# Kernel tuning notes

Hardware: AMD Instinct MI355X
Metric: run time of the kernel (lower is better)

The kernel has to match this reference:

```python
import jax, jax.numpy as jnp
import numpy as np

NUM_HEADS = 12


def setup_inputs() -> dict:
    key = jax.random.key(0)
    k1, k2, k3, k4 = jax.random.split(key, 4)
    dim = 768
    B, N1, N2 = 8, 64, 4096  # N1 must equal head_dim = dim // num_heads
    x = jax.random.normal(k1, (B, N1, dim), dtype=jnp.float32)
    y = jax.random.normal(k2, (B, N2, dim), dtype=jnp.float32)
    # torch nn.Linear layout: [out_features, in_features]
    W_qkv = jax.random.normal(k3, (3 * dim, dim), dtype=jnp.float32) * 0.02
    W_proj = jax.random.normal(k4, (dim, dim), dtype=jnp.float32) * 0.02
    b_proj = jnp.zeros((dim,), dtype=jnp.float32)
    return {"x": x, "y": y, "W_qkv": W_qkv, "W_proj": W_proj, "b_proj": b_proj}


def _split_heads(t, H):
    # [B, N, C] -> [B, H, N, C//H]
    B, N, C = t.shape
    return t.reshape(B, N, H, C // H).transpose(0, 2, 1, 3)


def reference(x, y, W_qkv, W_proj, b_proj):
    H = NUM_HEADS
    B1, N1, C = x.shape
    B2, N2, _ = y.shape
    hd = C // H
    scale = hd ** -0.5

    # qkv projections (bias=False); take q from x, k/v from y
    qkv_x = x @ W_qkv.T                      # [B, N1, 3C]
    q = _split_heads(qkv_x[..., :C], H)      # [B, H, N1, hd]
    qkv_y = y @ W_qkv.T                      # [B, N2, 3C]
    k = _split_heads(qkv_y[..., C:2 * C], H)  # [B, H, N2, hd]
    v = _split_heads(qkv_y[..., 2 * C:], H)   # [B, H, N2, hd]

    attn = jnp.einsum('bhqd,bhkd->bhqk', q, k) * scale  # [B, H, N1, N2]
    attn = jax.nn.softmax(attn, axis=-1)
    attn_t = attn.transpose(0, 1, 3, 2)       # [B, H, N2, N1]; N1 == hd

    # non-standard elementwise combine with v (requires N1 == hd)
    out = attn_t * v                          # [B, H, N2, hd]
    out = out.transpose(0, 2, 1, 3).reshape(B2, N2, C)
    return out @ W_proj.T + b_proj
```

## Files before the change

### kernel.cpp

```cpp
#include <hip/hip_runtime.h>
#include <math.h>


typedef __attribute__((ext_vector_type(8))) short short8;
typedef __attribute__((ext_vector_type(4))) float f32x4;

__device__ __forceinline__ ushort f2bf(float x) {
  unsigned u = __float_as_uint(x);
  u += 0x7fffu + ((u >> 16) & 1u);
  return (ushort)(u >> 16);
}
__device__ __forceinline__ float bf2f(ushort h) {
  return __uint_as_float((unsigned)h << 16);
}

__device__ __forceinline__ void gl_lds16(const ushort* g, ushort* l) {
  __builtin_amdgcn_global_load_lds(
      (__attribute__((address_space(1))) void*)g,
      (__attribute__((address_space(3))) void*)l, 16, 0, 0);
}

__global__ __launch_bounds__(256) void cast_all(
    const float* __restrict__ x, ushort* __restrict__ xb,
    const float* __restrict__ w1, ushort* __restrict__ w1b,
    const float* __restrict__ w2, ushort* __restrict__ w2b,
    const float* __restrict__ y, ushort* __restrict__ yb) {
  long i = (long)(blockIdx.x * 256 + threadIdx.x) * 8;
  if (i >= 27918336L) return;
  const float* s; ushort* d; long off;
  if (i < 393216L)        { s = x;  d = xb;  off = i; }
  else if (i < 2162688L)  { s = w1; d = w1b; off = i - 393216L; }
  else if (i < 2752512L)  { s = w2; d = w2b; off = i - 2162688L; }
  else                    { s = y;  d = yb;  off = i - 2752512L; }
  float4 a = *(const float4*)(s + off);
  float4 b = *(const float4*)(s + off + 4);
  ushort o[8] = {f2bf(a.x), f2bf(a.y), f2bf(a.z), f2bf(a.w),
                 f2bf(b.x), f2bf(b.y), f2bf(b.z), f2bf(b.w)};
  *(uint4*)(d + off) = *(const uint4*)o;
}

template <typename CT>
__device__ __forceinline__ void gemm8_body(
    const ushort* __restrict__ A, int lda,
    const ushort* __restrict__ B, int ldb,
    CT* __restrict__ C, int ldc,
    const float* __restrict__ bias, int rt, int ct)
{
  constexpr int NK = 12;
  __shared__ __align__(16) ushort Abuf[2][16384];
  __shared__ __align__(16) ushort Bbuf[2][16384];
  const int tid = threadIdx.x;
  const int m0 = rt * 256, n0 = ct * 256;
  const int wv = tid >> 6, lane = tid & 63;
  const int lm = lane & 15, quad = lane >> 4;
  const int WR = (wv >> 2) * 128, WC = (wv & 3) * 64;

  const int srow = lane >> 3;
  const int sg = (lane & 7) ^ srow;
  const ushort* Ag[4];
  const ushort* Bg[4];
#pragma unroll
  for (int j = 0; j < 4; ++j) {
    const int r = (wv * 4 + j) * 8 + srow;
    Ag[j] = A + (size_t)(m0 + r) * lda + sg * 8;
    Bg[j] = B + (size_t)(n0 + r) * ldb + sg * 8;
  }

  f32x4 acc[8][4];
#pragma unroll
  for (int i = 0; i < 8; ++i)
#pragma unroll
    for (int j = 0; j < 4; ++j) acc[i][j] = (f32x4)(0.f);

#pragma unroll
  for (int j = 0; j < 4; ++j) gl_lds16(Ag[j], &Abuf[0][(wv * 4 + j) * 512]);
#pragma unroll
  for (int j = 0; j < 4; ++j) gl_lds16(Bg[j], &Bbuf[0][(wv * 4 + j) * 512]);
#pragma unroll
  for (int j = 0; j < 4; ++j) gl_lds16(Bg[j] + 64, &Bbuf[1][(wv * 4 + j) * 512]);
  asm volatile("s_waitcnt vmcnt(4)" ::: "memory");
  __builtin_amdgcn_s_barrier();

#pragma unroll 1
  for (int T = 0; T < NK; ++T) {
    const ushort* Ab = &Abuf[T & 1][0];
    const ushort* Bb = &Bbuf[T & 1][0];
    ushort* An = &Abuf[(T & 1) ^ 1][0];
    ushort* Bn = &Bbuf[T & 1][0];
    const int k1 = (T + 1) * 64, k2 = (T + 2) * 64;
    const bool stA = (T + 1 < NK), stB = (T + 2 < NK);
    short8 bfr[4][2];

#pragma unroll
    for (int q = 0; q < 4; ++q) {
      if (q == 0) {
#pragma unroll
        for (int n = 0; n < 4; ++n)
#pragma unroll
          for (int ks = 0; ks < 2; ++ks)
            bfr[n][ks] = *(const short8*)(const void*)(
                Bb + (WC + n * 16 + lm) * 64 + ((ks * 4 + quad) ^ (lm & 7)) * 8);
      }
      short8 af[2][2];
#pragma unroll
      for (int i = 0; i < 2; ++i)
#pragma unroll
        for (int ks = 0; ks < 2; ++ks)
          af[i][ks] = *(const short8*)(const void*)(
              Ab + (WR + (q * 2 + i) * 16 + lm) * 64 + ((ks * 4 + quad) ^ (lm & 7)) * 8);
      if (q == 0 && stA) { gl_lds16(Ag[0] + k1, An + (wv * 4 + 0) * 512);
                           gl_lds16(Ag[1] + k1, An + (wv * 4 + 1) * 512); }
      if (q == 1 && stA) { gl_lds16(Ag[2] + k1, An + (wv * 4 + 2) * 512);
                           gl_lds16(Ag[3] + k1, An + (wv * 4 + 3) * 512); }
      if (q == 2 && stB) { gl_lds16(Bg[0] + k2, Bn + (wv * 4 + 0) * 512);
                           gl_lds16(Bg[1] + k2, Bn + (wv * 4 + 1) * 512); }
      if (q == 3 && stB) { gl_lds16(Bg[2] + k2, Bn + (wv * 4 + 2) * 512);
                           gl_lds16(Bg[3] + k2, Bn + (wv * 4 + 3) * 512); }
      __builtin_amdgcn_s_barrier();
      __builtin_amdgcn_s_setprio(1);
#pragma unroll
      for (int i = 0; i < 2; ++i)
#pragma unroll
        for (int n = 0; n < 4; ++n)
#pragma unroll
          for (int ks = 0; ks < 2; ++ks)
            acc[q * 2 + i][n] = __builtin_amdgcn_mfma_f32_16x16x32_bf16(
                af[i][ks], bfr[n][ks], acc[q * 2 + i][n], 0, 0, 0);
      __builtin_amdgcn_s_setprio(0);
      if (q == 3) {
        if (stB) asm volatile("s_waitcnt vmcnt(4)" ::: "memory");
        else     asm volatile("s_waitcnt vmcnt(0)" ::: "memory");
      }
      __builtin_amdgcn_s_barrier();
    }
  }
  __syncthreads();

  if constexpr (sizeof(CT) == 2) {
    ushort* eb = ((ushort*)&Abuf[0][0]) + wv * 2048;
#pragma unroll
    for (int i = 0; i < 8; ++i) {
      ushort* ebc = eb + (i & 1) * 1024;
#pragma unroll
      for (int j = 0; j < 4; ++j)
#pragma unroll
        for (int r = 0; r < 4; ++r) {
          const int R = quad * 4 + r;
          const int gt = j * 2 + (lm >> 3);
          const int gs = (gt + R) & 7;
          ebc[R * 64 + gs * 8 + (lm & 7)] = f2bf(acc[i][j][r]);
        }
#pragma unroll
      for (int p = 0; p < 2; ++p) {
        const int R2 = (lane >> 3) + p * 8;
        const int g = lane & 7;
        const int gt2 = (g - R2) & 7;
        uint4 v = *(const uint4*)(const void*)(ebc + R2 * 64 + g * 8);
        *(uint4*)(C + (size_t)(m0 + WR + i * 16 + R2) * ldc + n0 + WC + gt2 * 8) = v;
      }
    }
  } else {
#pragma unroll
    for (int j = 0; j < 4; ++j) {
      const int col = n0 + WC + j * 16 + lm;
      const float bb = bias ? bias[col] : 0.f;
#pragma unroll
      for (int i = 0; i < 8; ++i) {
        const int row = m0 + WR + i * 16 + quad * 4;
#pragma unroll
        for (int r = 0; r < 4; ++r)
          C[(size_t)(row + r) * ldc + col] = (CT)(acc[i][j][r] + bb);
      }
    }
  }
}

__global__ __launch_bounds__(512, 2) void kv_gemm8(
    const ushort* __restrict__ ybf, const ushort* __restrict__ wkv,
    ushort* __restrict__ kvbf)
{
  const int id = blockIdx.x;
  const int xcd = id & 7, local = id >> 3;
  const int rt = xcd * 16 + (local & 15);
  const int ct = local >> 4;
  gemm8_body<ushort>(ybf, 768, wkv, 768, kvbf, 1536, nullptr, rt, ct);
}

__global__ __launch_bounds__(512, 2) void out_gemm8(
    const ushort* __restrict__ Ebf, const ushort* __restrict__ wpbf,
    const float* __restrict__ bias, float* __restrict__ out)
{
  const int id = blockIdx.x;
  const int xcd = id & 7, local = id >> 3;
  const int rt = xcd * 16 + (local & 15);
  const int ct = local >> 4;
  gemm8_body<float>(Ebf, 768, wpbf, 768, out, 768, bias, rt, ct);
}

__global__ __launch_bounds__(256) void q_gemm(
    const ushort* __restrict__ A, const ushort* __restrict__ B,
    ushort* __restrict__ C)
{
  constexpr int lda = 768, ldb = 768, ldc = 768, K = 768;
  __shared__ __align__(16) ushort As[2][4096];
  __shared__ __align__(16) ushort Bs[2][4096];
  const int tid = threadIdx.x;
  const int rt = blockIdx.x & 3, ct = blockIdx.x >> 2;
  const int m0 = rt * 128, n0 = ct * 128;

  const int w = tid >> 6, lane = tid & 63;
  const int lm = lane & 15, quad = lane >> 4;
  const int wm = (w & 1) * 64, wn = (w >> 1) * 64;

  const int G0 = w * 64 + lane, G1 = G0 + 256;
  const int r0 = G0 >> 2, c0 = ((G0 & 3) - (r0 >> 1)) & 3;
  const int r1 = G1 >> 2, c1 = ((G1 & 3) - (r1 >> 1)) & 3;
  const ushort* Ag0 = A + (size_t)(m0 + r0) * lda + c0 * 8;
  const ushort* Ag1 = A + (size_t)(m0 + r1) * lda + c1 * 8;
  const ushort* Bg0 = B + (size_t)(n0 + r0) * ldb + c0 * 8;
  const ushort* Bg1 = B + (size_t)(n0 + r1) * ldb + c1 * 8;
  const int lds0 = w * 512, lds1 = w * 512 + 2048;

  f32x4 acc[4][4];
#pragma unroll
  for (int i = 0; i < 4; ++i)
#pragma unroll
    for (int j = 0; j < 4; ++j) acc[i][j] = (f32x4)(0.f);

  const int nk = K >> 5;
  gl_lds16(Ag0, &As[0][lds0]); gl_lds16(Ag1, &As[0][lds1]);
  gl_lds16(Bg0, &Bs[0][lds0]); gl_lds16(Bg1, &Bs[0][lds1]);

  int cur = 0;
  for (int kk = 0; kk < nk; ++kk) {
    __syncthreads();
    if (kk + 1 < nk) {
      const int k0 = (kk + 1) << 5;
      gl_lds16(Ag0 + k0, &As[cur ^ 1][lds0]); gl_lds16(Ag1 + k0, &As[cur ^ 1][lds1]);
      gl_lds16(Bg0 + k0, &Bs[cur ^ 1][lds0]); gl_lds16(Bg1 + k0, &Bs[cur ^ 1][lds1]);
    }
    const ushort* Ab = &As[cur][0];
    const ushort* Bb = &Bs[cur][0];
    short8 af[4], bf8[4];
#pragma unroll
    for (int i = 0; i < 4; ++i) {
      const int Ra = wm + i * 16 + lm;
      af[i] = *(const short8*)(const void*)(Ab + Ra * 32 + ((quad + (Ra >> 1)) & 3) * 8);
      const int Rb = wn + i * 16 + lm;
      bf8[i] = *(const short8*)(const void*)(Bb + Rb * 32 + ((quad + (Rb >> 1)) & 3) * 8);
    }
#pragma unroll
    for (int i = 0; i < 4; ++i)
#pragma unroll
      for (int j = 0; j < 4; ++j)
        acc[i][j] = __builtin_amdgcn_mfma_f32_16x16x32_bf16(af[i], bf8[j], acc[i][j], 0, 0, 0);
    cur ^= 1;
  }
  __syncthreads();

  ushort* eb = ((ushort*)&Bs[0][0]) + w * 2048;
#pragma unroll
  for (int i = 0; i < 4; ++i) {
    ushort* ebc = eb + (i & 1) * 1024;
#pragma unroll
    for (int j = 0; j < 4; ++j)
#pragma unroll
      for (int r = 0; r < 4; ++r) {
        const int R = quad * 4 + r;
        const int gt = j * 2 + (lm >> 3);
        const int gs = (gt + R) & 7;
        ebc[R * 64 + gs * 8 + (lm & 7)] = f2bf(acc[i][j][r]);
      }
#pragma unroll
    for (int p = 0; p < 2; ++p) {
      const int R2 = (lane >> 3) + p * 8;
      const int g = lane & 7;
      const int gt2 = (g - R2) & 7;
      uint4 v = *(const uint4*)(const void*)(ebc + R2 * 64 + g * 8);
      *(uint4*)(C + (size_t)(m0 + wm + i * 16 + R2) * ldc + n0 + wn + gt2 * 8) = v;
    }
  }
}

__global__ __launch_bounds__(256) void attn_pass1(
    const ushort* __restrict__ Q,
    const ushort* __restrict__ KV,
    float* __restrict__ parts)
{
  const int chunk = blockIdx.x, h = blockIdx.y, b = blockIdx.z;
  const int tid = threadIdx.x;
  __shared__ __align__(16) ushort Qs[64 * 72];
  __shared__ __align__(16) ushort Ks[128 * 72];
  __shared__ float sm[4][64], ss[4][64];
#pragma unroll
  for (int p = 0; p < 2; ++p) {
    const int G = tid + 256 * p, row = G >> 3, g = G & 7;
    *(uint4*)(Qs + row * 72 + g * 8) =
        *(const uint4*)(Q + (size_t)(b * 64 + row) * 768 + h * 64 + g * 8);
  }
#pragma unroll
  for (int p = 0; p < 4; ++p) {
    const int G = tid + 256 * p, row = G >> 3, g = G & 7;
    *(uint4*)(Ks + row * 72 + g * 8) =
        *(const uint4*)(KV + (size_t)(b * 4096 + chunk * 128 + row) * 1536 + h * 64 + g * 8);
  }
  __syncthreads();

  const int w = tid >> 6, lane = tid & 63;
  const int lm = lane & 15, quad = lane >> 4;
  const int wn = w * 32;

  f32x4 acc[4][2];
#pragma unroll
  for (int i = 0; i < 4; ++i) { acc[i][0] = (f32x4)(0.f); acc[i][1] = (f32x4)(0.f); }
#pragma unroll
  for (int s = 0; s < 2; ++s) {
    short8 qf[4], kf[2];
#pragma unroll
    for (int i = 0; i < 4; ++i)
      qf[i] = *(const short8*)(const void*)(Qs + (i * 16 + lm) * 72 + s * 32 + quad * 8);
#pragma unroll
    for (int jn = 0; jn < 2; ++jn)
      kf[jn] = *(const short8*)(const void*)(Ks + (wn + jn * 16 + lm) * 72 + s * 32 + quad * 8);
#pragma unroll
    for (int i = 0; i < 4; ++i)
#pragma unroll
      for (int jn = 0; jn < 2; ++jn)
        acc[i][jn] = __builtin_amdgcn_mfma_f32_16x16x32_bf16(qf[i], kf[jn], acc[i][jn], 0, 0, 0);
  }

#pragma unroll
  for (int i = 0; i < 4; ++i)
#pragma unroll
    for (int r = 0; r < 4; ++r) {
      float v0 = acc[i][0][r] * 0.125f, v1 = acc[i][1][r] * 0.125f;
      float m = fmaxf(v0, v1);
      m = fmaxf(m, __shfl_xor(m, 1)); m = fmaxf(m, __shfl_xor(m, 2));
      m = fmaxf(m, __shfl_xor(m, 4)); m = fmaxf(m, __shfl_xor(m, 8));
      float e = __expf(v0 - m) + __expf(v1 - m);
      e += __shfl_xor(e, 1); e += __shfl_xor(e, 2);
      e += __shfl_xor(e, 4); e += __shfl_xor(e, 8);
      if (lm == 0) {
        const int j = i * 16 + quad * 4 + r;
        sm[w][j] = m; ss[w][j] = e;
      }
    }
  __syncthreads();
  if (tid < 64) {
    float g = fmaxf(fmaxf(sm[0][tid], sm[1][tid]), fmaxf(sm[2][tid], sm[3][tid]));
    float s = ss[0][tid] * __expf(sm[0][tid] - g) + ss[1][tid] * __expf(sm[1][tid] - g)
            + ss[2][tid] * __expf(sm[2][tid] - g) + ss[3][tid] * __expf(sm[3][tid] - g);
    const int bh = b * 12 + h;
    float* p = parts + ((size_t)(bh * 32 + chunk) * 64 + tid) * 2;
    p[0] = g; p[1] = s;
  }
}

__global__ __launch_bounds__(256) void attn_pass2(
    const ushort* __restrict__ Q, const ushort* __restrict__ KV,
    const float* __restrict__ parts, ushort* __restrict__ E)
{
  const int chunk = blockIdx.x, h = blockIdx.y, b = blockIdx.z;
  const int tid = threadIdx.x;
  __shared__ __align__(16) ushort Qs[64 * 72];
  __shared__ __align__(16) ushort Ks[128 * 72];
  __shared__ __align__(16) ushort Vs[128 * 72];
  __shared__ float st[64][2];
#pragma unroll
  for (int p = 0; p < 2; ++p) {
    const int G = tid + 256 * p, row = G >> 3, g = G & 7;
    *(uint4*)(Qs + row * 72 + g * 8) =
        *(const uint4*)(Q + (size_t)(b * 64 + row) * 768 + h * 64 + g * 8);
  }
#pragma unroll
  for (int p = 0; p < 4; ++p) {
    const int G = tid + 256 * p, row = G >> 3, g = G & 7;
    const size_t rbase = (size_t)(b * 4096 + chunk * 128 + row) * 1536 + h * 64 + g * 8;
    *(uint4*)(Ks + row * 72 + g * 8) = *(const uint4*)(KV + rbase);
    *(uint4*)(Vs + row * 72 + g * 8) = *(const uint4*)(KV + rbase + 768);
  }
  {
    const int bh = b * 12 + h;
    const int tq = tid >> 2, tc = tid & 3;
    float pm[8], ps[8];
    float gm = -1e30f;
#pragma unroll
    for (int c = 0; c < 8; ++c) {
      const float* p = parts + ((size_t)(bh * 32 + tc * 8 + c) * 64 + tq) * 2;
      pm[c] = p[0]; ps[c] = p[1];
      gm = fmaxf(gm, pm[c]);
    }
    gm = fmaxf(gm, __shfl_xor(gm, 1));
    gm = fmaxf(gm, __shfl_xor(gm, 2));
    float s = 0.f;
#pragma unroll
    for (int c = 0; c < 8; ++c) s += ps[c] * __expf(pm[c] - gm);
    s += __shfl_xor(s, 1);
    s += __shfl_xor(s, 2);
    if (tc == 0) { st[tq][0] = gm; st[tq][1] = 1.f / s; }
  }
  __syncthreads();

  const int w = tid >> 6, lane = tid & 63;
  const int lm = lane & 15, quad = lane >> 4;
  const int wn = w * 32;

  f32x4 acc[4][2];
#pragma unroll
  for (int i = 0; i < 4; ++i) { acc[i][0] = (f32x4)(0.f); acc[i][1] = (f32x4)(0.f); }
#pragma unroll
  for (int s = 0; s < 2; ++s) {
    short8 qf[4], kf[2];
#pragma unroll
    for (int i = 0; i < 4; ++i)
      qf[i] = *(const short8*)(const void*)(Qs + (i * 16 + lm) * 72 + s * 32 + quad * 8);
#pragma unroll
    for (int jn = 0; jn < 2; ++jn)
      kf[jn] = *(const short8*)(const void*)(Ks + (wn + jn * 16 + lm) * 72 + s * 32 + quad * 8);
#pragma unroll
    for (int i = 0; i < 4; ++i)
#pragma unroll
      for (int jn = 0; jn < 2; ++jn)
        acc[i][jn] = __builtin_amdgcn_mfma_f32_16x16x32_bf16(qf[i], kf[jn], acc[i][jn], 0, 0, 0);
  }

  ushort ev[4][2][4];
#pragma unroll
  for (int i = 0; i < 4; ++i)
#pragma unroll
    for (int jn = 0; jn < 2; ++jn)
#pragma unroll
      for (int r = 0; r < 4; ++r) {
        const float v = acc[i][jn][r] * 0.125f;
        const int j = i * 16 + quad * 4 + r;
        const float p = __expf(v - st[j][0]) * st[j][1];
        const int key = wn + jn * 16 + lm;
        ev[i][jn][r] = f2bf(p * bf2f(Vs[key * 72 + j]));
      }
  __syncthreads();
  ushort* Es = Ks;
#pragma unroll
  for (int i = 0; i < 4; ++i)
#pragma unroll
    for (int jn = 0; jn < 2; ++jn)
#pragma unroll
      for (int r = 0; r < 4; ++r)
        Es[(wn + jn * 16 + lm) * 72 + i * 16 + quad * 4 + r] = ev[i][jn][r];
  __syncthreads();
#pragma unroll
  for (int k = 0; k < 4; ++k) {
    const int row = tid >> 1, g = (tid & 1) * 4 + k;
    uint4 v = *(const uint4*)(const void*)(Es + row * 72 + g * 8);
    *(uint4*)(E + (size_t)(b * 4096 + chunk * 128 + row) * 768 + h * 64 + g * 8) = v;
  }
}

extern "C" void kernel_launch(void* const* d_in, const int* in_sizes, int n_in,
                              void* d_out, int out_size, void* d_ws, size_t ws_size,
                              hipStream_t stream) {
  const float* x     = (const float*)d_in[0];
  const float* y     = (const float*)d_in[1];
  const float* Wqkv  = (const float*)d_in[2];
  const float* Wproj = (const float*)d_in[3];
  const float* bproj = (const float*)d_in[4];
  float* out = (float*)d_out;

  char* wsb = (char*)d_ws;
  ushort* xbf    = (ushort*)(wsb + 0);
  ushort* qbf    = (ushort*)(wsb + 786432);
  ushort* wqkvbf = (ushort*)(wsb + 1572864);
  float*  parts  = (float*)(wsb + 1572864);
  ushort* wpbf   = (ushort*)(wsb + 5111808);
  ushort* ybf    = (ushort*)(wsb + 6291456);
  ushort* Ebf    = ybf;
  ushort* KVbf   = (ushort*)(wsb + 56623104);

  cast_all<<<13632, 256, 0, stream>>>(x, xbf, Wqkv, wqkvbf, Wproj, wpbf, y, ybf);

  q_gemm<<<24, 256, 0, stream>>>(xbf, wqkvbf, qbf);

  kv_gemm8<<<768, 512, 0, stream>>>(ybf, wqkvbf + (size_t)768 * 768, KVbf);

  attn_pass1<<<dim3(32, 12, 8), 256, 0, stream>>>(qbf, KVbf, parts);
  attn_pass2<<<dim3(32, 12, 8), 256, 0, stream>>>(qbf, KVbf, parts, Ebf);

  out_gemm8<<<384, 512, 0, stream>>>(Ebf, wpbf, bproj, out);
}
```

Baseline: 413.3 us.

## Compute unnormalized attention outputs in pass1, rescale afterwards instead of recomputing QK

Pass 1 now also loads V, computes exp(s - chunk_max) times V immediately, and stores the result as fp16 into the E buffer. A lightweight rescale kernel then applies exp(chunk_max - global_max)/sum per query column and converts to bf16 in place. This removes the second QK^T computation and the second read of K, V and Q in pass 2. In exchange E is written and read one extra time, and precision depends on fp16 holding the unnormalized values.

```diff
diff --git a/kernel.cpp b/kernel.cpp
--- a/kernel.cpp
+++ b/kernel.cpp
@@ -1,4 +1,5 @@
 #include <hip/hip_runtime.h>
+#include <hip/hip_fp16.h>
 #include <math.h>
 
 
@@ -12,6 +13,14 @@
 }
 __device__ __forceinline__ float bf2f(ushort h) {
   return __uint_as_float((unsigned)h << 16);
+}
+__device__ __forceinline__ ushort f2h(float x) {
+  __half h = __float2half(x);
+  return *reinterpret_cast<ushort*>(&h);
+}
+__device__ __forceinline__ float h2f(ushort u) {
+  __half h = *reinterpret_cast<__half*>(&u);
+  return __half2float(h);
 }
 
 __device__ __forceinline__ void gl_lds16(const ushort* g, ushort* l) {
@@ -285,13 +294,15 @@
 __global__ __launch_bounds__(256) void attn_pass1(
     const ushort* __restrict__ Q,
     const ushort* __restrict__ KV,
-    float* __restrict__ parts)
+    float* __restrict__ parts,
+    ushort* __restrict__ Ep)
 {
   const int chunk = blockIdx.x, h = blockIdx.y, b = blockIdx.z;
   const int tid = threadIdx.x;
   __shared__ __align__(16) ushort Qs[64 * 72];
   __shared__ __align__(16) ushort Ks[128 * 72];
-  __shared__ float sm[4][64], ss[4][64];
+  __shared__ __align__(16) ushort Vs[128 * 72];
+  __shared__ float sm[4][64], ss[4][64], gmx[64];
 #pragma unroll
   for (int p = 0; p < 2; ++p) {
     const int G = tid + 256 * p, row = G >> 3, g = G & 7;
@@ -301,8 +312,9 @@
 #pragma unroll
   for (int p = 0; p < 4; ++p) {
     const int G = tid + 256 * p, row = G >> 3, g = G & 7;
-    *(uint4*)(Ks + row * 72 + g * 8) =
-        *(const uint4*)(KV + (size_t)(b * 4096 + chunk * 128 + row) * 1536 + h * 64 + g * 8);
+    const size_t rbase = (size_t)(b * 4096 + chunk * 128 + row) * 1536 + h * 64 + g * 8;
+    *(uint4*)(Ks + row * 72 + g * 8) = *(const uint4*)(KV + rbase);
+    *(uint4*)(Vs + row * 72 + g * 8) = *(const uint4*)(KV + rbase + 768);
   }
   __syncthreads();
 
@@ -353,32 +365,46 @@
     const int bh = b * 12 + h;
     float* p = parts + ((size_t)(bh * 32 + chunk) * 64 + tid) * 2;
     p[0] = g; p[1] = s;
-  }
-}
-
-__global__ __launch_bounds__(256) void attn_pass2(
-    const ushort* __restrict__ Q, const ushort* __restrict__ KV,
-    const float* __restrict__ parts, ushort* __restrict__ E)
+    gmx[tid] = g;
+  }
+  __syncthreads();
+
+  ushort ev[4][2][4];
+#pragma unroll
+  for (int i = 0; i < 4; ++i)
+#pragma unroll
+    for (int jn = 0; jn < 2; ++jn)
+#pragma unroll
+      for (int r = 0; r < 4; ++r) {
+        const float v = acc[i][jn][r] * 0.125f;
+        const int j = i * 16 + quad * 4 + r;
+        const float p = __expf(v - gmx[j]);
+        const int key = wn + jn * 16 + lm;
+        ev[i][jn][r] = f2h(p * bf2f(Vs[key * 72 + j]));
+      }
+  ushort* Es = Ks;
+#pragma unroll
+  for (int i = 0; i < 4; ++i)
+#pragma unroll
+    for (int jn = 0; jn < 2; ++jn)
+#pragma unroll
+      for (int r = 0; r < 4; ++r)
+        Es[(wn + jn * 16 + lm) * 72 + i * 16 + quad * 4 + r] = ev[i][jn][r];
+  __syncthreads();
+#pragma unroll
+  for (int k = 0; k < 4; ++k) {
+    const int row = tid >> 1, g = (tid & 1) * 4 + k;
+    uint4 v = *(const uint4*)(const void*)(Es + row * 72 + g * 8);
+    *(uint4*)(Ep + (size_t)(b * 4096 + chunk * 128 + row) * 768 + h * 64 + g * 8) = v;
+  }
+}
+
+__global__ __launch_bounds__(256) void attn_rescale(
+    const float* __restrict__ parts, ushort* E)
 {
   const int chunk = blockIdx.x, h = blockIdx.y, b = blockIdx.z;
   const int tid = threadIdx.x;
-  __shared__ __align__(16) ushort Qs[64 * 72];
-  __shared__ __align__(16) ushort Ks[128 * 72];
-  __shared__ __align__(16) ushort Vs[128 * 72];
-  __shared__ float st[64][2];
-#pragma unroll
-  for (int p = 0; p < 2; ++p) {
-    const int G = tid + 256 * p, row = G >> 3, g = G & 7;
-    *(uint4*)(Qs + row * 72 + g * 8) =
-        *(const uint4*)(Q + (size_t)(b * 64 + row) * 768 + h * 64 + g * 8);
-  }
-#pragma unroll
-  for (int p = 0; p < 4; ++p) {
-    const int G = tid + 256 * p, row = G >> 3, g = G & 7;
-    const size_t rbase = (size_t)(b * 4096 + chunk * 128 + row) * 1536 + h * 64 + g * 8;
-    *(uint4*)(Ks + row * 72 + g * 8) = *(const uint4*)(KV + rbase);
-    *(uint4*)(Vs + row * 72 + g * 8) = *(const uint4*)(KV + rbase + 768);
-  }
+  __shared__ float sc[64];
   {
     const int bh = b * 12 + h;
     const int tq = tid >> 2, tc = tid & 3;
@@ -397,61 +423,24 @@
     for (int c = 0; c < 8; ++c) s += ps[c] * __expf(pm[c] - gm);
     s += __shfl_xor(s, 1);
     s += __shfl_xor(s, 2);
-    if (tc == 0) { st[tq][0] = gm; st[tq][1] = 1.f / s; }
-  }
-  __syncthreads();
-
-  const int w = tid >> 6, lane = tid & 63;
-  const int lm = lane & 15, quad = lane >> 4;
-  const int wn = w * 32;
-
-  f32x4 acc[4][2];
-#pragma unroll
-  for (int i = 0; i < 4; ++i) { acc[i][0] = (f32x4)(0.f); acc[i][1] = (f32x4)(0.f); }
-#pragma unroll
-  for (int s = 0; s < 2; ++s) {
-    short8 qf[4], kf[2];
-#pragma unroll
-    for (int i = 0; i < 4; ++i)
-      qf[i] = *(const short8*)(const void*)(Qs + (i * 16 + lm) * 72 + s * 32 + quad * 8);
-#pragma unroll
-    for (int jn = 0; jn < 2; ++jn)
-      kf[jn] = *(const short8*)(const void*)(Ks + (wn + jn * 16 + lm) * 72 + s * 32 + quad * 8);
-#pragma unroll
-    for (int i = 0; i < 4; ++i)
-#pragma unroll
-      for (int jn = 0; jn < 2; ++jn)
-        acc[i][jn] = __builtin_amdgcn_mfma_f32_16x16x32_bf16(qf[i], kf[jn], acc[i][jn], 0, 0, 0);
-  }
-
-  ushort ev[4][2][4];
-#pragma unroll
-  for (int i = 0; i < 4; ++i)
-#pragma unroll
-    for (int jn = 0; jn < 2; ++jn)
-#pragma unroll
-      for (int r = 0; r < 4; ++r) {
-        const float v = acc[i][jn][r] * 0.125f;
-        const int j = i * 16 + quad * 4 + r;
-        const float p = __expf(v - st[j][0]) * st[j][1];
-        const int key = wn + jn * 16 + lm;
-        ev[i][jn][r] = f2bf(p * bf2f(Vs[key * 72 + j]));
-      }
-  __syncthreads();
-  ushort* Es = Ks;
-#pragma unroll
-  for (int i = 0; i < 4; ++i)
-#pragma unroll
-    for (int jn = 0; jn < 2; ++jn)
-#pragma unroll
-      for (int r = 0; r < 4; ++r)
-        Es[(wn + jn * 16 + lm) * 72 + i * 16 + quad * 4 + r] = ev[i][jn][r];
-  __syncthreads();
+    if (tc == 0) {
+      const float mc = parts[((size_t)(bh * 32 + chunk) * 64 + tq) * 2];
+      sc[tq] = __expf(mc - gm) / s;
+    }
+  }
+  __syncthreads();
+  const size_t base = (size_t)(b * 4096 + chunk * 128 + (tid >> 1)) * 768
+                    + h * 64 + (tid & 1) * 32;
+  const int c0 = (tid & 1) * 32;
 #pragma unroll
   for (int k = 0; k < 4; ++k) {
-    const int row = tid >> 1, g = (tid & 1) * 4 + k;
-    uint4 v = *(const uint4*)(const void*)(Es + row * 72 + g * 8);
-    *(uint4*)(E + (size_t)(b * 4096 + chunk * 128 + row) * 768 + h * 64 + g * 8) = v;
+    uint4 v = *(const uint4*)(E + base + k * 8);
+    const ushort* pv = (const ushort*)&v;
+    ushort o[8];
+#pragma unroll
+    for (int e = 0; e < 8; ++e)
+      o[e] = f2bf(h2f(pv[e]) * sc[c0 + k * 8 + e]);
+    *(uint4*)(E + base + k * 8) = *(const uint4*)o;
   }
 }
 
@@ -481,8 +470,8 @@
 
   kv_gemm8<<<768, 512, 0, stream>>>(ybf, wqkvbf + (size_t)768 * 768, KVbf);
 
-  attn_pass1<<<dim3(32, 12, 8), 256, 0, stream>>>(qbf, KVbf, parts);
-  attn_pass2<<<dim3(32, 12, 8), 256, 0, stream>>>(qbf, KVbf, parts, Ebf);
+  attn_pass1<<<dim3(32, 12, 8), 256, 0, stream>>>(qbf, KVbf, parts, Ebf);
+  attn_rescale<<<dim3(32, 12, 8), 256, 0, stream>>>(parts, Ebf);
 
   out_gemm8<<<384, 512, 0, stream>>>(Ebf, wpbf, bproj, out);
 }
```

Result: slower. 435.8 us (+5.4%).
